# Kernel optimization log

Measured on AMD Instinct MI355X. Metric: run time of the kernel, lower is better.

Reference implementation:

```python
import jax, jax.numpy as jnp
import numpy as np


def setup_inputs() -> dict:
    key = jax.random.key(0)
    k1, k2, k3 = jax.random.split(key, 3)
    B, C, T, V, M = 16, 256, 256, 25, 2
    O = 128  # dim2
    x = jax.random.normal(k1, (B, C, T, V, M), dtype=jnp.float32)
    # Conv3d 1x1, bias=False -> weight [out_ch, in_ch]
    W1 = jax.random.normal(k2, (O, C), dtype=jnp.float32) * (1.0 / np.sqrt(C))
    W2 = jax.random.normal(k3, (O, C), dtype=jnp.float32) * (1.0 / np.sqrt(C))
    return {"x": x, "W1": W1, "W2": W2}


def reference(x, W1, W2):
    # x: [B, C, T, V, M]; 1x1 Conv3d == channel GEMM
    s1 = jnp.einsum('bctvm,oc->botvm', x, W1)  # [B, O, T, V, M]
    s2 = jnp.einsum('bctvm,oc->botvm', x, W2)  # [B, O, T, V, M]
    # s1.permute(0,4,3,2,1) -> [B,M,V,T,O]; s2.permute(0,4,3,1,2) -> [B,M,V,O,T]
    # matmul -> scores [B, M, V, T, T], contracted over O
    s3 = jnp.einsum('botvm,bosvm->bmvts', s1, s2)
    return jax.nn.softmax(s3, axis=-1)
```

## Files before the change

kernel.cpp:

```cpp
#include <hip/hip_runtime.h>
#include <math.h>


#define C_DIM 256
#define T_DIM 256
#define V_DIM 25
#define M_DIM 2
#define O_DIM 128
#define O2    (O_DIM * 2)
#define N_DIM (T_DIM * V_DIM * M_DIM)
#define VM    (V_DIM * M_DIM)
#define KC    32

__global__ __launch_bounds__(256)
void stage1_gemm(const float* __restrict__ x, const float* __restrict__ W1,
                 const float* __restrict__ W2, float* __restrict__ ws, int b0) {
    const int b  = b0 + blockIdx.z;
    const int vm = blockIdx.y;
    const int t0 = blockIdx.x * 64;
    const float* xb = x + (size_t)b * C_DIM * N_DIM;
    float* outv = ws + ((size_t)blockIdx.z * VM + vm) * ((size_t)O2 * T_DIM);

    __shared__ float Wt[KC][260];
    __shared__ float Xt[KC][68];

    const int tid = threadIdx.x;

    const int wo = tid;
    const float* wrow = (wo < O_DIM) ? (W1 + (size_t)wo * C_DIM)
                                     : (W2 + (size_t)(wo - O_DIM) * C_DIM);
    const int xt  = tid & 63;
    const int xkb = (tid >> 6) * 8;

    const int to = tid >> 3;
    const int tt = tid & 7;

    float acc[8][8] = {};

    for (int kc = 0; kc < C_DIM; kc += KC) {
        float4 wv[8];
        #pragma unroll
        for (int j = 0; j < 8; j++)
            wv[j] = *(const float4*)&wrow[kc + 4 * j];
        float xv[8];
        #pragma unroll
        for (int j = 0; j < 8; j++)
            xv[j] = xb[(size_t)(kc + xkb + j) * N_DIM + (size_t)(t0 + xt) * VM + vm];

        __syncthreads();
        #pragma unroll
        for (int j = 0; j < 8; j++) {
            Wt[4 * j + 0][wo] = wv[j].x;
            Wt[4 * j + 1][wo] = wv[j].y;
            Wt[4 * j + 2][wo] = wv[j].z;
            Wt[4 * j + 3][wo] = wv[j].w;
        }
        #pragma unroll
        for (int j = 0; j < 8; j++)
            Xt[xkb + j][xt] = xv[j];
        __syncthreads();

        #pragma unroll 4
        for (int k = 0; k < KC; k++) {
            float4 a0 = *(const float4*)&Wt[k][to * 8];
            float4 a1 = *(const float4*)&Wt[k][to * 8 + 4];
            float4 b0 = *(const float4*)&Xt[k][tt * 4];
            float4 b1 = *(const float4*)&Xt[k][tt * 4 + 32];
            float a[8]  = {a0.x, a0.y, a0.z, a0.w, a1.x, a1.y, a1.z, a1.w};
            float bv[8] = {b0.x, b0.y, b0.z, b0.w, b1.x, b1.y, b1.z, b1.w};
            #pragma unroll
            for (int i = 0; i < 8; i++)
                #pragma unroll
                for (int j = 0; j < 8; j++)
                    acc[i][j] = fmaf(a[i], bv[j], acc[i][j]);
        }
    }

    #pragma unroll
    for (int i = 0; i < 8; i++) {
        float* row = outv + (size_t)(to * 8 + i) * T_DIM + t0;
        float4 r0 = {acc[i][0], acc[i][1], acc[i][2], acc[i][3]};
        float4 r1 = {acc[i][4], acc[i][5], acc[i][6], acc[i][7]};
        *(float4*)&row[tt * 4]      = r0;
        *(float4*)&row[tt * 4 + 32] = r1;
    }
}

__global__ __launch_bounds__(512)
void stage2_softmax(const float* __restrict__ ws, float* __restrict__ out, int b0) {
    const int bl = blockIdx.z;
    const int b  = b0 + bl;
    const int vm = blockIdx.y;
    const int t0 = blockIdx.x * 64;
    const float* s12b = ws + ((size_t)bl * VM + vm) * ((size_t)O2 * T_DIM);
    const float* s1 = s12b;
    const float* s2 = s12b + (size_t)O_DIM * T_DIM;

    __shared__ float At[32][68];
    __shared__ float Bt[32][260];

    const int tid = threadIdx.x;
    const int ty = tid >> 5;
    const int tx = tid & 31;

    const int lr = tid >> 4;
    const int lt = (tid & 15) * 4;
    const int ls = (tid & 15) * 16;

    float acc[4][8] = {};

    for (int kc = 0; kc < O_DIM; kc += 32) {
        float4 av  = *(const float4*)&s1[(size_t)(kc + lr) * T_DIM + t0 + lt];
        float4 bv0 = *(const float4*)&s2[(size_t)(kc + lr) * T_DIM + ls];
        float4 bv1 = *(const float4*)&s2[(size_t)(kc + lr) * T_DIM + ls + 4];
        float4 bv2 = *(const float4*)&s2[(size_t)(kc + lr) * T_DIM + ls + 8];
        float4 bv3 = *(const float4*)&s2[(size_t)(kc + lr) * T_DIM + ls + 12];
        __syncthreads();
        *(float4*)&At[lr][lt]      = av;
        *(float4*)&Bt[lr][ls]      = bv0;
        *(float4*)&Bt[lr][ls + 4]  = bv1;
        *(float4*)&Bt[lr][ls + 8]  = bv2;
        *(float4*)&Bt[lr][ls + 12] = bv3;
        __syncthreads();

        #pragma unroll 2
        for (int k = 0; k < 32; k++) {
            float4 a  = *(const float4*)&At[k][ty * 4];
            float4 b0 = *(const float4*)&Bt[k][tx * 8];
            float4 b1 = *(const float4*)&Bt[k][tx * 8 + 4];
            float av_[4] = {a.x, a.y, a.z, a.w};
            float bv_[8] = {b0.x, b0.y, b0.z, b0.w, b1.x, b1.y, b1.z, b1.w};
            #pragma unroll
            for (int i = 0; i < 4; i++)
                #pragma unroll
                for (int j = 0; j < 8; j++)
                    acc[i][j] = fmaf(av_[i], bv_[j], acc[i][j]);
        }
    }

    const int mm = vm & 1;
    const int vv = vm >> 1;
    const size_t rowbase0 = (((size_t)b * M_DIM + mm) * V_DIM + vv) * T_DIM;

    #pragma unroll
    for (int i = 0; i < 4; i++) {
        float mx = -INFINITY;
        #pragma unroll
        for (int j = 0; j < 8; j++) mx = fmaxf(mx, acc[i][j]);
        #pragma unroll
        for (int d = 16; d >= 1; d >>= 1) mx = fmaxf(mx, __shfl_xor(mx, d));
        float p[8];
        float l = 0.f;
        #pragma unroll
        for (int j = 0; j < 8; j++) { p[j] = __expf(acc[i][j] - mx); l += p[j]; }
        #pragma unroll
        for (int d = 16; d >= 1; d >>= 1) l += __shfl_xor(l, d);
        const float inv = 1.0f / l;
        float4 r0 = {p[0] * inv, p[1] * inv, p[2] * inv, p[3] * inv};
        float4 r1 = {p[4] * inv, p[5] * inv, p[6] * inv, p[7] * inv};
        float* orow = out + (rowbase0 + t0 + ty * 4 + i) * T_DIM + tx * 8;
        *(float4*)orow       = r0;
        *((float4*)orow + 1) = r1;
    }
}

extern "C" void kernel_launch(void* const* d_in, const int* in_sizes, int n_in,
                              void* d_out, int out_size, void* d_ws, size_t ws_size,
                              hipStream_t stream) {
    const float* x  = (const float*)d_in[0];
    const float* W1 = (const float*)d_in[1];
    const float* W2 = (const float*)d_in[2];
    float* out = (float*)d_out;
    float* ws  = (float*)d_ws;

    const size_t per_b_bytes = (size_t)VM * O2 * T_DIM * sizeof(float);
    int nb = (int)(ws_size / per_b_bytes);
    if (nb < 1) return;
    if (nb > 16) nb = 16;

    for (int b0 = 0; b0 < 16; b0 += nb) {
        const int n = (16 - b0 < nb) ? (16 - b0) : nb;
        stage1_gemm<<<dim3(T_DIM / 64, VM, n), 256, 0, stream>>>(x, W1, W2, ws, b0);
        stage2_softmax<<<dim3(T_DIM / 64, VM, n), 512, 0, stream>>>(ws, out, b0);
    }
}
```

Before: 859.5 us.

## Use split-fp16 MFMA for the stage-1 channel GEMM with prefetched x

Stage 1 now splits the weights and the x tile into high and low fp16 parts and accumulates three 16x16x32 fp16 MFMA products per tile, approximating fp32 precision on matrix cores instead of scalar FMA. A small prep kernel converts the weights once per call into a workspace tail. The next x chunk is prefetched into registers while the current one is computed. The aim is to cut stage-1 compute time, at the cost of slightly lower precision and a smaller workspace for batching.

```diff
diff --git a/kernel.cpp b/kernel.cpp
--- a/kernel.cpp
+++ b/kernel.cpp
@@ -10,79 +10,107 @@
 #define O2    (O_DIM * 2)
 #define N_DIM (T_DIM * V_DIM * M_DIM)
 #define VM    (V_DIM * M_DIM)
-#define KC    32
+
+typedef _Float16 half8 __attribute__((ext_vector_type(8)));
+typedef float f32x4 __attribute__((ext_vector_type(4)));
 
 __global__ __launch_bounds__(256)
-void stage1_gemm(const float* __restrict__ x, const float* __restrict__ W1,
-                 const float* __restrict__ W2, float* __restrict__ ws, int b0) {
+void prep_w(const float* __restrict__ W1, const float* __restrict__ W2,
+            _Float16* __restrict__ Wh, _Float16* __restrict__ Wl) {
+    const int o2 = blockIdx.x;
+    const int c  = threadIdx.x;
+    const float w = (o2 < O_DIM) ? W1[(size_t)o2 * C_DIM + c]
+                                 : W2[(size_t)(o2 - O_DIM) * C_DIM + c];
+    const _Float16 h = (_Float16)w;
+    Wh[(size_t)o2 * C_DIM + c] = h;
+    Wl[(size_t)o2 * C_DIM + c] = (_Float16)(w - (float)h);
+}
+
+__global__ __launch_bounds__(256)
+void stage1_gemm(const float* __restrict__ x,
+                 const _Float16* __restrict__ Wh, const _Float16* __restrict__ Wl,
+                 float* __restrict__ ws, int b0) {
     const int b  = b0 + blockIdx.z;
     const int vm = blockIdx.y;
     const int t0 = blockIdx.x * 64;
     const float* xb = x + (size_t)b * C_DIM * N_DIM;
     float* outv = ws + ((size_t)blockIdx.z * VM + vm) * ((size_t)O2 * T_DIM);
 
-    __shared__ float Wt[KC][260];
-    __shared__ float Xt[KC][68];
-
-    const int tid = threadIdx.x;
-
-    const int wo = tid;
-    const float* wrow = (wo < O_DIM) ? (W1 + (size_t)wo * C_DIM)
-                                     : (W2 + (size_t)(wo - O_DIM) * C_DIM);
+    __shared__ __attribute__((aligned(16))) _Float16 Bh[64][40];
+    __shared__ __attribute__((aligned(16))) _Float16 Bl[64][40];
+
+    const int tid  = threadIdx.x;
+    const int lane = tid & 63;
+    const int wv   = tid >> 6;
+    const int l15  = lane & 15;
+    const int lg   = lane >> 4;
+
     const int xt  = tid & 63;
     const int xkb = (tid >> 6) * 8;
-
-    const int to = tid >> 3;
-    const int tt = tid & 7;
-
-    float acc[8][8] = {};
-
-    for (int kc = 0; kc < C_DIM; kc += KC) {
-        float4 wv[8];
-        #pragma unroll
-        for (int j = 0; j < 8; j++)
-            wv[j] = *(const float4*)&wrow[kc + 4 * j];
-        float xv[8];
-        #pragma unroll
-        for (int j = 0; j < 8; j++)
-            xv[j] = xb[(size_t)(kc + xkb + j) * N_DIM + (size_t)(t0 + xt) * VM + vm];
-
-        __syncthreads();
+    const float* xcol = xb + (size_t)(t0 + xt) * VM + vm;
+
+    const size_t wbase = (size_t)(wv * 64 + l15) * C_DIM + 8 * lg;
+
+    f32x4 acc[4][4] = {};
+
+    float xv[8];
+    #pragma unroll
+    for (int j = 0; j < 8; j++)
+        xv[j] = xcol[(size_t)(xkb + j) * N_DIM];
+
+    for (int kc = 0; kc < C_DIM; kc += 32) {
+        half8 hv, lv;
         #pragma unroll
         for (int j = 0; j < 8; j++) {
-            Wt[4 * j + 0][wo] = wv[j].x;
-            Wt[4 * j + 1][wo] = wv[j].y;
-            Wt[4 * j + 2][wo] = wv[j].z;
-            Wt[4 * j + 3][wo] = wv[j].w;
-        }
-        #pragma unroll
-        for (int j = 0; j < 8; j++)
-            Xt[xkb + j][xt] = xv[j];
-        __syncthreads();
-
-        #pragma unroll 4
-        for (int k = 0; k < KC; k++) {
-            float4 a0 = *(const float4*)&Wt[k][to * 8];
-            float4 a1 = *(const float4*)&Wt[k][to * 8 + 4];
-            float4 b0 = *(const float4*)&Xt[k][tt * 4];
-            float4 b1 = *(const float4*)&Xt[k][tt * 4 + 32];
-            float a[8]  = {a0.x, a0.y, a0.z, a0.w, a1.x, a1.y, a1.z, a1.w};
-            float bv[8] = {b0.x, b0.y, b0.z, b0.w, b1.x, b1.y, b1.z, b1.w};
-            #pragma unroll
-            for (int i = 0; i < 8; i++)
-                #pragma unroll
-                for (int j = 0; j < 8; j++)
-                    acc[i][j] = fmaf(a[i], bv[j], acc[i][j]);
-        }
+            const _Float16 h = (_Float16)xv[j];
+            hv[j] = h;
+            lv[j] = (_Float16)(xv[j] - (float)h);
+        }
+        __syncthreads();
+        *(half8*)&Bh[xt][xkb] = hv;
+        *(half8*)&Bl[xt][xkb] = lv;
+
+        if (kc + 32 < C_DIM) {
+            #pragma unroll
+            for (int j = 0; j < 8; j++)
+                xv[j] = xcol[(size_t)(kc + 32 + xkb + j) * N_DIM];
+        }
+
+        half8 ah[4], al[4];
+        #pragma unroll
+        for (int i = 0; i < 4; i++) {
+            const size_t wrow = wbase + (size_t)i * 16 * C_DIM + kc;
+            ah[i] = *(const half8*)(Wh + wrow);
+            al[i] = *(const half8*)(Wl + wrow);
+        }
+        __syncthreads();
+
+        half8 bh[4], bl[4];
+        #pragma unroll
+        for (int j = 0; j < 4; j++) {
+            bh[j] = *(const half8*)&Bh[j * 16 + l15][8 * lg];
+            bl[j] = *(const half8*)&Bl[j * 16 + l15][8 * lg];
+        }
+
+        #pragma unroll
+        for (int i = 0; i < 4; i++)
+            #pragma unroll
+            for (int j = 0; j < 4; j++) {
+                acc[i][j] = __builtin_amdgcn_mfma_f32_16x16x32_f16(ah[i], bh[j], acc[i][j], 0, 0, 0);
+                acc[i][j] = __builtin_amdgcn_mfma_f32_16x16x32_f16(ah[i], bl[j], acc[i][j], 0, 0, 0);
+                acc[i][j] = __builtin_amdgcn_mfma_f32_16x16x32_f16(al[i], bh[j], acc[i][j], 0, 0, 0);
+            }
     }
 
     #pragma unroll
-    for (int i = 0; i < 8; i++) {
-        float* row = outv + (size_t)(to * 8 + i) * T_DIM + t0;
-        float4 r0 = {acc[i][0], acc[i][1], acc[i][2], acc[i][3]};
-        float4 r1 = {acc[i][4], acc[i][5], acc[i][6], acc[i][7]};
-        *(float4*)&row[tt * 4]      = r0;
-        *(float4*)&row[tt * 4 + 32] = r1;
+    for (int i = 0; i < 4; i++) {
+        #pragma unroll
+        for (int j = 0; j < 4; j++) {
+            float* p = outv + (size_t)(wv * 64 + i * 16 + lg * 4) * T_DIM + t0 + j * 16 + l15;
+            #pragma unroll
+            for (int r = 0; r < 4; r++)
+                p[(size_t)r * T_DIM] = acc[i][j][r];
+        }
     }
 }
 
@@ -174,13 +202,21 @@
     float* ws  = (float*)d_ws;
 
     const size_t per_b_bytes = (size_t)VM * O2 * T_DIM * sizeof(float);
-    int nb = (int)(ws_size / per_b_bytes);
+    const size_t wtail = 2 * (size_t)O2 * C_DIM * sizeof(_Float16);
+    if (ws_size < wtail + per_b_bytes) return;
+    const size_t wsplit_off = (ws_size - wtail) & ~(size_t)255;
+    _Float16* Whp = (_Float16*)((char*)ws + wsplit_off);
+    _Float16* Wlp = Whp + (size_t)O2 * C_DIM;
+
+    int nb = (int)(wsplit_off / per_b_bytes);
     if (nb < 1) return;
     if (nb > 16) nb = 16;
 
+    prep_w<<<dim3(O2), C_DIM, 0, stream>>>(W1, W2, Whp, Wlp);
+
     for (int b0 = 0; b0 < 16; b0 += nb) {
         const int n = (16 - b0 < nb) ? (16 - b0) : nb;
-        stage1_gemm<<<dim3(T_DIM / 64, VM, n), 256, 0, stream>>>(x, W1, W2, ws, b0);
+        stage1_gemm<<<dim3(T_DIM / 64, VM, n), 256, 0, stream>>>(x, Whp, Wlp, ws, b0);
         stage2_softmax<<<dim3(T_DIM / 64, VM, n), 512, 0, stream>>>(ws, out, b0);
     }
 }
```

New measurement: 787.8 us. 1.09x faster.
